# Performance work log

Measured on AMD Instinct MI355X. Metric: run time of the kernel, lower is better.

Reference implementation:

```python
import jax, jax.numpy as jnp
import numpy as np

B, TZ, TU = 32, 16, 128
E, H, V = 512, 1024, 32000
FREQ_THRES = 4   # cfg.freq_thres: zero out copy prob for most-frequent tokens
LN_EPS = 1e-3


def setup_inputs() -> dict:
    key = jax.random.key(0)
    ks = jax.random.split(key, 16)
    s = lambda k, shape, sc=0.02: jax.random.normal(k, shape, jnp.float32) * sc
    return dict(
        z_enc_out=jax.random.normal(ks[0], (TZ, B, H), jnp.float32),
        pz_proba=jax.nn.softmax(jax.random.normal(ks[1], (TZ, B, V), jnp.float32), axis=-1),
        u_enc_out=jax.random.normal(ks[2], (TU, B, H), jnp.float32),
        m_t_input=jax.random.randint(ks[3], (1, B), 0, V),
        last_hidden=jax.random.normal(ks[4], (1, B, H), jnp.float32),
        emb=s(ks[5], (V, E), 1.0 / np.sqrt(E)),
        Wa_z=s(ks[6], (2 * H, H)), ba_z=jnp.zeros((H,), jnp.float32), v_z=s(ks[7], (H,), 1.0 / np.sqrt(H)),
        Wa_u=s(ks[8], (2 * H, H)), ba_u=jnp.zeros((H,), jnp.float32), v_u=s(ks[9], (H,), 1.0 / np.sqrt(H)),
        W_ih=s(ks[10], (3 * H, E + 2 * H)), W_hh=s(ks[11], (3 * H, H)),
        b_ih=jnp.zeros((3 * H,), jnp.float32), b_hh=jnp.zeros((3 * H,), jnp.float32),
        ln_a=jnp.ones((H,), jnp.float32), ln_b=jnp.zeros((H,), jnp.float32),
        W_proj=s(ks[12], (H, V)), b_proj=jnp.zeros((V,), jnp.float32),
        W_c=s(ks[13], (2 * H, H)), b_c=jnp.zeros((H,), jnp.float32),
        W_v1=s(ks[14], (H, 1)), b_v1=jnp.zeros((1,), jnp.float32),
    )


def _attn(hidden, enc, Wa, ba, v):
    # hidden [1,B,H], enc [T,B,H] -> context [1,B,H]
    hh = jnp.broadcast_to(hidden, enc.shape)                       # [T,B,H]
    energy = jnp.tanh(jnp.concatenate([hh, enc], -1) @ Wa + ba)    # [T,B,H]
    scores = jnp.einsum('tbh,h->bt', energy, v)                    # [B,T]
    w = jax.nn.softmax(scores, axis=1)
    return jnp.einsum('bt,tbh->bh', w, enc)[None]                  # [1,B,H]


def _layernorm(x, a, b):
    mu = jnp.mean(x, axis=-1, keepdims=True)
    sigma = jnp.std(x, axis=-1, keepdims=True, ddof=1)  # torch.std is unbiased
    return (x - mu) / (sigma + LN_EPS) * a + b


def reference(z_enc_out, pz_proba, u_enc_out, m_t_input, last_hidden,
              emb, Wa_z, ba_z, v_z, Wa_u, ba_u, v_u,
              W_ih, W_hh, b_ih, b_hh, ln_a, ln_b,
              W_proj, b_proj, W_c, b_c, W_v1, b_v1):
    m_embed = emb[m_t_input]                                       # [1,B,E]
    z_ctx = _attn(last_hidden, z_enc_out, Wa_z, ba_z, v_z)         # [1,B,H]
    u_ctx = _attn(last_hidden, u_enc_out, Wa_u, ba_u, v_u)         # [1,B,H]
    x = jnp.concatenate([z_ctx, u_ctx, m_embed], -1)[0]            # [B,2H+E]
    h = last_hidden[0]                                             # [B,H]
    # single-step GRU (torch gate order: r, z, n)
    gi = x @ W_ih.T + b_ih
    gh = h @ W_hh.T + b_hh
    ir, iz, inn = jnp.split(gi, 3, axis=-1)
    hr, hz, hn = jnp.split(gh, 3, axis=-1)
    r = jax.nn.sigmoid(ir + hr)
    zg = jax.nn.sigmoid(iz + hz)
    n = jnp.tanh(inn + r * hn)
    h_new = (1.0 - zg) * n + zg * h                                # [B,H]
    gru_out = _layernorm(h_new, ln_a, ln_b)                        # [B,H]
    gen_score = gru_out @ W_proj + b_proj                          # [B,V]
    # tanh-linear copy score over z positions
    g_rep = jnp.broadcast_to(gru_out[None], z_enc_out.shape)       # [Tz,B,H]
    zc = jnp.tanh(jnp.concatenate([z_enc_out, g_rep], -1) @ W_c + b_c)  # [Tz,B,H]
    zc = (zc @ W_v1 + b_v1)[..., 0].T                              # [B,Tz]
    # joint softmax over [gen | copy]
    scores = jax.nn.softmax(jnp.concatenate([gen_score, zc], axis=1), axis=1)
    gen_p, copy_p = scores[:, :V], scores[:, V:]
    copy_v = jnp.einsum('bt,tbv->bv', copy_p, pz_proba)            # mask_prob bmm
    freq_mask = (jnp.arange(V) >= FREQ_THRES).astype(gen_p.dtype)
    proba = gen_p + copy_v * freq_mask
    return proba, h_new[None]
```

## Files before the change

kernel.cpp:

```cpp
#include <hip/hip_runtime.h>
#include <stdint.h>

#define B_ 32
#define TZ_ 16
#define TU_ 128
#define E_ 512
#define H_ 1024
#define V_ 32000
#define X_ 2560
#define H3_ 3072
#define LN_EPS_ 0.001f

#define NP_IH 20
#define NP_HH 16

typedef unsigned short ushort_t;
typedef ushort_t us4 __attribute__((ext_vector_type(4)));
typedef ushort_t us8 __attribute__((ext_vector_type(8)));
typedef short bf16x8 __attribute__((ext_vector_type(8)));
typedef float f32x4 __attribute__((ext_vector_type(4)));

__device__ __forceinline__ float bf2f(ushort_t u){
  union { unsigned int i; float f; } x; x.i = ((unsigned int)u) << 16; return x.f;
}
__device__ __forceinline__ ushort_t f2b(float f){
  union { float f; unsigned int i; } u; u.f = f;
  unsigned int x = u.i;
  return (ushort_t)((x + 0x7fffu + ((x >> 16) & 1u)) >> 16);
}
__device__ __forceinline__ bool is_bf(const void* lnA){
  return *(const unsigned int*)lnA == 0x3F803F80u;
}
__device__ __forceinline__ float ldg_(const void* p, size_t i, bool isb){
  return isb ? bf2f(((const ushort_t*)p)[i]) : ((const float*)p)[i];
}
__device__ __forceinline__ float sigm(float x){ return 1.0f/(1.0f + __expf(-x)); }
__device__ __forceinline__ float tanh_f(float x){
  float cx = fminf(fmaxf(x, -9.0f), 9.0f);
  float t = __expf(2.0f*cx);
  return (t - 1.0f)/(t + 1.0f);
}

__global__ void k0_init(const void* lh, const void* emb, const int* mt,
                        const void* ba_z, const void* ba_u, const void* b_c, const void* bpj,
                        const void* lnA,
                        float* h_f32, ushort_t* hb, float* x, float* hWaZ, float* hWaU,
                        float* sz, float* su, float* gruWc, float* genscore){
  bool isb = is_bf(lnA);
  int i = blockIdx.x*256 + threadIdx.x;
  if (i < 32768){ float v = ldg_(lh, i, isb); h_f32[i] = v; hb[i] = f2b(v); return; }
  i -= 32768;
  if (i < 16384){ int b = i >> 9, e = i & 511;
    x[b*X_ + 2048 + e] = ldg_(emb, (size_t)(unsigned)mt[b]*E_ + e, isb); return; }
  i -= 16384;
  if (i < 32768){ hWaZ[i] = ldg_(ba_z, i & 1023, isb); return; }
  i -= 32768;
  if (i < 32768){ hWaU[i] = ldg_(ba_u, i & 1023, isb); return; }
  i -= 32768;
  if (i < 4608){ if (i < 512) sz[i] = 0.f; else su[i-512] = 0.f; return; }
  i -= 4608;
  if (i < 32768){ gruWc[i] = ldg_(b_c, i & 1023, isb); return; }
  i -= 32768;
  if (i < 1024000){
    int b = i / V_;
    int v = i - b*V_;
    genscore[(size_t)b*V_ + v] = ldg_(bpj, v, isb);
    return;
  }
}

__global__ void kC_cvt(const void* uenc, const void* zenc, const void* Wih, const void* Whh,
                       const void* lnA,
                       ushort_t* uB, ushort_t* zB, ushort_t* WihB, ushort_t* WhhB){
  bool isb = is_bf(lnA);
  long long i = (long long)(blockIdx.x*256 + threadIdx.x) * 8;
  const long long NU = (long long)TU_*B_*H_;
  const long long NZ = (long long)TZ_*B_*H_;
  const long long NI = (long long)H3_*X_;
  const long long NH = (long long)H3_*H_;
  const void* src; ushort_t* dst;
  if (i < NU){ src = uenc; dst = uB; }
  else if ((i -= NU) < NZ){ src = zenc; dst = zB; }
  else if ((i -= NZ) < NI){ src = Wih; dst = WihB; }
  else if ((i -= NI) < NH){ src = Whh; dst = WhhB; }
  else return;
  if (isb){
    *(us8*)&dst[i] = *(const us8*)((const ushort_t*)src + i);
  } else {
    const float* s = (const float*)src + i;
    float4 a0 = *(const float4*)s, a1 = *(const float4*)(s + 4);
    us8 o;
    o[0]=f2b(a0.x); o[1]=f2b(a0.y); o[2]=f2b(a0.z); o[3]=f2b(a0.w);
    o[4]=f2b(a1.x); o[5]=f2b(a1.y); o[6]=f2b(a1.z); o[7]=f2b(a1.w);
    *(us8*)&dst[i] = o;
  }
}

__global__ void kX_cvt(const float* x, ushort_t* xb){
  int i = (blockIdx.x*256 + threadIdx.x) * 8;
  const float* s = x + i;
  float4 a0 = *(const float4*)s, a1 = *(const float4*)(s + 4);
  us8 o;
  o[0]=f2b(a0.x); o[1]=f2b(a0.y); o[2]=f2b(a0.z); o[3]=f2b(a0.w);
  o[4]=f2b(a1.x); o[5]=f2b(a1.y); o[6]=f2b(a1.z); o[7]=f2b(a1.w);
  *(us8*)&xb[i] = o;
}

__global__ void kT_transpose(const void* Wz, const void* Wu, const void* Wc, const void* lnA,
                             ushort_t* tZ, ushort_t* tU, ushort_t* tC){
  bool isb = is_bf(lnA);
  int w = blockIdx.z;
  const void* src = (w==0)? Wz : (w==1)? Wu : Wc;
  size_t base = (w==2) ? 0 : (size_t)H_*H_;
  ushort_t* dst = (w==0)? tZ : (w==1)? tU : tC;
  __shared__ ushort_t T[64][68];
  int k0 = blockIdx.x*64, j0 = blockIdx.y*64;
  int tx = threadIdx.x & 15, ty = threadIdx.x >> 4;
  if (isb){
    const ushort_t* s = (const ushort_t*)src + base;
    #pragma unroll
    for (int rr=0; rr<4; ++rr){
      int row = ty + rr*16;
      *(us4*)&T[row][tx*4] = *(const us4*)&s[(size_t)(k0+row)*H_ + j0 + tx*4];
    }
  } else {
    const float* s = (const float*)src + base;
    #pragma unroll
    for (int rr=0; rr<4; ++rr){
      int row = ty + rr*16;
      #pragma unroll
      for (int c=0;c<4;c++)
        T[row][tx*4+c] = f2b(s[(size_t)(k0+row)*H_ + j0 + tx*4 + c]);
    }
  }
  __syncthreads();
  #pragma unroll
  for (int rr=0; rr<4; ++rr){
    int row = ty + rr*16;
    us4 o;
    o[0]=T[tx*4+0][row]; o[1]=T[tx*4+1][row]; o[2]=T[tx*4+2][row]; o[3]=T[tx*4+3][row];
    *(us4*)&dst[(size_t)(j0+row)*H_ + k0 + tx*4] = o;
  }
}

__global__ void k1_kj(const float* xf, const void* W0, const void* W1, int eloff, const void* lnA,
                      float* out0, float* out1){
  bool isb = is_bf(lnA);
  const void* W = blockIdx.z ? W1 : W0;
  float* out = blockIdx.z ? out1 : out0;
  int j = blockIdx.x*256 + threadIdx.x;
  int k0v = blockIdx.y*64;
  float acc[32];
  #pragma unroll
  for (int b=0;b<32;b++) acc[b]=0.f;
  if (isb){
    const ushort_t* Wp = (const ushort_t*)W + eloff;
    #pragma unroll 4
    for (int k=k0v; k<k0v+64; ++k){
      float w = bf2f(Wp[(size_t)k*H_ + j]);
      #pragma unroll
      for (int b=0;b<32;b++) acc[b] = fmaf(xf[b*H_ + k], w, acc[b]);
    }
  } else {
    const float* Wp = (const float*)W + eloff;
    #pragma unroll 4
    for (int k=k0v; k<k0v+64; ++k){
      float w = Wp[(size_t)k*H_ + j];
      #pragma unroll
      for (int b=0;b<32;b++) acc[b] = fmaf(xf[b*H_ + k], w, acc[b]);
    }
  }
  #pragma unroll
  for (int b=0;b<32;b++) unsafeAtomicAdd(&out[b*H_ + j], acc[b]);
}

__global__ __launch_bounds__(256) void k2_mfma(const ushort_t* Ab, const ushort_t* WB,
                                               float* part, int K, int kchunk){
  int j0 = blockIdx.x*128;
  int kb = blockIdx.y*kchunk;
  __shared__ ushort_t Bs[128*32];
  int tid = threadIdx.x, wid = tid >> 6, lane = tid & 63;
  int q = lane >> 4, n = lane & 15;
  int rrow = tid >> 2, t4 = tid & 3;
  f32x4 acc[2][2];
  #pragma unroll
  for (int r=0;r<2;r++)
    #pragma unroll
    for (int c=0;c<2;c++)
      #pragma unroll
      for (int e=0;e<4;e++) acc[r][c][e] = 0.f;

  for (int kt = 0; kt < kchunk; kt += 32){
    int k = kb + kt;
    __syncthreads();
    #pragma unroll
    for (int p=0;p<2;p++){
      const ushort_t* srcB = WB + (size_t)(j0 + p*64 + rrow)*K + k + t4*8;
      __builtin_amdgcn_global_load_lds(srcB, &Bs[(p*64 + wid*16)*32], 16, 0, 0);
    }
    __syncthreads();
    bf16x8 af[2], bfr[2];
    #pragma unroll
    for (int r=0;r<2;r++) af[r] = *(const bf16x8*)&Ab[(size_t)(r*16 + n)*K + k + q*8];
    #pragma unroll
    for (int c=0;c<2;c++) bfr[c] = *(const bf16x8*)&Bs[(wid*32 + c*16 + n)*32 + q*8];
    #pragma unroll
    for (int r=0;r<2;r++)
      #pragma unroll
      for (int c=0;c<2;c++)
        acc[r][c] = __builtin_amdgcn_mfma_f32_16x16x32_bf16(af[r], bfr[c], acc[r][c], 0, 0, 0);
  }
  int p = blockIdx.y;
  #pragma unroll
  for (int r=0;r<2;r++)
    #pragma unroll
    for (int c=0;c<2;c++)
      #pragma unroll
      for (int i=0;i<4;i++){
        int b = r*16 + q*4 + i;
        int j = j0 + wid*32 + c*16 + n;
        part[(size_t)(p*32 + b)*H3_ + j] = acc[r][c][i];
      }
}

__global__ __launch_bounds__(256) void k3_mfma(
    const ushort_t* uB, const ushort_t* zB,
    const ushort_t* tU, const ushort_t* tZ, const ushort_t* tC,
    const float* hWaU, const float* hWaZ,
    const void* v_u, const void* v_z, const void* lnA,
    float* su, float* sz, float* zcpre)
{
  bool isb = is_bf(lnA);
  int which = blockIdx.z;
  int bx = blockIdx.x, nt = blockIdx.y;
  int mt;
  const ushort_t* A; const ushort_t* BT;
  if (which == 0){ A = uB; BT = tU; mt = bx; }
  else {
    int lo = (which==1) ? 8 : 12;
    if (bx < lo || bx >= lo+4) return;
    mt = bx - lo;
    A = zB; BT = (which==1) ? tZ : tC;
  }
  __shared__ ushort_t As[128*32];
  __shared__ ushort_t Bs[64*32];
  int tid = threadIdx.x;
  int wid = tid >> 6, lane = tid & 63;
  int q = lane >> 4, n = lane & 15;
  int wm = wid & 1, wn = wid >> 1;
  int r0 = mt*128, j0 = nt*64;
  f32x4 acc[4][2];
  #pragma unroll
  for (int a=0;a<4;a++)
    #pragma unroll
    for (int c=0;c<2;c++)
      #pragma unroll
      for (int e=0;e<4;e++) acc[a][c][e] = 0.f;

  int rrow = tid >> 2, t4 = tid & 3;

  for (int kt = 0; kt < 32; ++kt){
    __syncthreads();
    #pragma unroll
    for (int p=0;p<2;p++){
      const ushort_t* srcA = A + (size_t)(r0 + p*64 + rrow)*H_ + kt*32 + t4*8;
      __builtin_amdgcn_global_load_lds(srcA, &As[(p*64 + wid*16)*32], 16, 0, 0);
    }
    {
      const ushort_t* srcB = BT + (size_t)(j0 + rrow)*H_ + kt*32 + t4*8;
      __builtin_amdgcn_global_load_lds(srcB, &Bs[(wid*16)*32], 16, 0, 0);
    }
    __syncthreads();
    bf16x8 af[4], bfr[2];
    #pragma unroll
    for (int f=0;f<4;f++) af[f] = *(const bf16x8*)&As[(wm*64 + f*16 + n)*32 + q*8];
    #pragma unroll
    for (int f=0;f<2;f++) bfr[f] = *(const bf16x8*)&Bs[(wn*32 + f*16 + n)*32 + q*8];
    #pragma unroll
    for (int fr=0;fr<4;fr++)
      #pragma unroll
      for (int fn=0;fn<2;fn++)
        acc[fr][fn] = __builtin_amdgcn_mfma_f32_16x16x32_bf16(af[fr], bfr[fn], acc[fr][fn], 0, 0, 0);
  }

  if (which < 2){
    const float* pre = (which==0) ? hWaU : hWaZ;
    const void* vv = (which==0) ? v_u : v_z;
    float* score = (which==0) ? su : sz;
    float s[4][4];
    #pragma unroll
    for (int fr=0;fr<4;fr++)
      #pragma unroll
      for (int i=0;i<4;i++) s[fr][i]=0.f;
    #pragma unroll
    for (int fr=0;fr<4;fr++){
      #pragma unroll
      for (int fn=0;fn<2;fn++){
        int j  = j0 + wn*32 + fn*16 + n;
        float vj = ldg_(vv, j, isb);
        #pragma unroll
        for (int i=0;i<4;i++){
          int rl = wm*64 + fr*16 + q*4 + i;
          int b  = rl & 31;
          s[fr][i] += tanh_f(acc[fr][fn][i] + pre[b*H_ + j]) * vj;
        }
      }
    }
    #pragma unroll
    for (int fr=0;fr<4;fr++)
      #pragma unroll
      for (int i=0;i<4;i++){
        float t = s[fr][i];
        t += __shfl_xor(t, 1);
        t += __shfl_xor(t, 2);
        t += __shfl_xor(t, 4);
        t += __shfl_xor(t, 8);
        if (n == 0){
          int rl = wm*64 + fr*16 + q*4 + i;
          unsafeAtomicAdd(&score[r0 + rl], t);
        }
      }
  } else {
    #pragma unroll
    for (int fr=0;fr<4;fr++)
      #pragma unroll
      for (int fn=0;fn<2;fn++)
        #pragma unroll
        for (int i=0;i<4;i++){
          int rl = wm*64 + fr*16 + q*4 + i;
          int jl = wn*32 + fn*16 + n;
          zcpre[(size_t)(r0 + rl)*H_ + j0 + jl] = acc[fr][fn][i];
        }
  }
}

__global__ void k4_ctx(const float* sz, const float* su,
                       const void* zenc, const void* uenc, const void* lnA, float* x){
  bool isb = is_bf(lnA);
  int jc = blockIdx.x, b = blockIdx.y, which = blockIdx.z;
  int T = which ? TU_ : TZ_;
  const float* sc = which ? su : sz;
  const void* enc = which ? uenc : zenc;
  __shared__ float red[256];
  __shared__ float w[TU_];
  int tid = threadIdx.x;
  float v = (tid < T) ? sc[tid*B_ + b] : -1e30f;
  red[tid] = v; __syncthreads();
  for (int s=128; s>0; s>>=1){ if (tid < s) red[tid] = fmaxf(red[tid], red[tid+s]); __syncthreads(); }
  float m = red[0]; __syncthreads();
  float e = (tid < T) ? __expf(v - m) : 0.f;
  red[tid] = e; __syncthreads();
  for (int s=128; s>0; s>>=1){ if (tid < s) red[tid] += red[tid+s]; __syncthreads(); }
  float S = red[0]; __syncthreads();
  if (tid < T) w[tid] = e / S;
  __syncthreads();
  int j = jc*256 + tid;
  float acc = 0.f;
  #pragma unroll 4
  for (int t=0; t<T; ++t) acc = fmaf(w[t], ldg_(enc, (size_t)(t*B_ + b)*H_ + j, isb), acc);
  x[b*X_ + which*H_ + j] = acc;
}

__global__ __launch_bounds__(1024) void k5_gru(const float* gip, const float* ghp,
                       const void* b_ih, const void* b_hh,
                       const void* lh, const void* ln_a, const void* ln_b,
                       float* gru, float* hout){
  bool isb = is_bf(ln_a);
  int b = blockIdx.x, tid = threadIdx.x;
  __shared__ float red[1024];
  int j = tid;
  float ir = ldg_(b_ih, j, isb), iz = ldg_(b_ih, 1024+j, isb), inn = ldg_(b_ih, 2048+j, isb);
  float hr = ldg_(b_hh, j, isb), hz = ldg_(b_hh, 1024+j, isb), hn = ldg_(b_hh, 2048+j, isb);
  #pragma unroll 4
  for (int p=0;p<NP_IH;p++){
    const float* gp = &gip[(size_t)(p*32 + b)*H3_];
    ir += gp[j]; iz += gp[1024+j]; inn += gp[2048+j];
  }
  #pragma unroll 4
  for (int p=0;p<NP_HH;p++){
    const float* gp = &ghp[(size_t)(p*32 + b)*H3_];
    hr += gp[j]; hz += gp[1024+j]; hn += gp[2048+j];
  }
  float hv = ldg_(lh, b*H_ + j, isb);
  float r  = sigm(ir + hr);
  float zg = sigm(iz + hz);
  float nn = tanh_f(inn + r*hn);
  float h2 = (1.f - zg)*nn + zg*hv;
  hout[b*H_ + j] = h2;
  red[tid] = h2; __syncthreads();
  for (int s=512;s>0;s>>=1){ if(tid<s) red[tid]+=red[tid+s]; __syncthreads(); }
  float mu = red[0] / 1024.f; __syncthreads();
  red[tid] = h2*h2; __syncthreads();
  for (int s=512;s>0;s>>=1){ if(tid<s) red[tid]+=red[tid+s]; __syncthreads(); }
  float var = (red[0] - 1024.f*mu*mu) / 1023.f;
  float sg = sqrtf(fmaxf(var, 0.f));
  float inv = 1.f/(sg + LN_EPS_);
  gru[b*H_ + j] = (h2 - mu)*inv*ldg_(ln_a, j, isb) + ldg_(ln_b, j, isb);
}

__global__ void k7_zc(const float* zcpre, const float* gruWc, const void* Wv1,
                      const void* b_v1, const void* lnA, float* zc){
  bool isb = is_bf(lnA);
  int r = blockIdx.x, b = r & 31, tid = threadIdx.x;
  __shared__ float red[256];
  float s = 0.f;
  #pragma unroll
  for (int jj=0;jj<4;jj++){
    int j = tid + jj*256;
    float e = tanh_f(zcpre[(size_t)r*H_ + j] + gruWc[b*H_ + j]);
    s = fmaf(e, ldg_(Wv1, j, isb), s);
  }
  red[tid] = s; __syncthreads();
  for (int st=128;st>0;st>>=1){ if(tid<st) red[tid]+=red[tid+st]; __syncthreads(); }
  if (tid==0) zc[r] = red[0] + ldg_(b_v1, 0, isb);
}

__global__ __launch_bounds__(256) void k6_proj(const float* gru, const void* Wp,
                                               const void* lnA, float* genscore){
  bool isb = is_bf(lnA);
  int v = blockIdx.x*256 + threadIdx.x;
  int h0 = blockIdx.y*128;
  float acc[32];
  #pragma unroll
  for (int b=0;b<32;b++) acc[b]=0.f;
  if (isb){
    const ushort_t* W = (const ushort_t*)Wp;
    #pragma unroll 4
    for (int h=h0; h<h0+128; ++h){
      float w = bf2f(W[(size_t)h*V_ + v]);
      #pragma unroll
      for (int b=0;b<32;b++) acc[b] = fmaf(gru[b*H_ + h], w, acc[b]);
    }
  } else {
    const float* W = (const float*)Wp;
    #pragma unroll 4
    for (int h=h0; h<h0+128; ++h){
      float w = W[(size_t)h*V_ + v];
      #pragma unroll
      for (int b=0;b<32;b++) acc[b] = fmaf(gru[b*H_ + h], w, acc[b]);
    }
  }
  #pragma unroll
  for (int b=0;b<32;b++) unsafeAtomicAdd(&genscore[(size_t)b*V_ + v], acc[b]);
}

__global__ void k8a(const float* genscore, float* statpart){
  int v = blockIdx.x*256 + threadIdx.x;
  int b = blockIdx.y, tid = threadIdx.x;
  __shared__ float red[256];
  float g = genscore[(size_t)b*V_ + v];
  red[tid] = g; __syncthreads();
  for (int s=128;s>0;s>>=1){ if(tid<s) red[tid]=fmaxf(red[tid],red[tid+s]); __syncthreads(); }
  float m = red[0]; __syncthreads();
  float e = __expf(g - m);
  red[tid] = e; __syncthreads();
  for (int s=128;s>0;s>>=1){ if(tid<s) red[tid]+=red[tid+s]; __syncthreads(); }
  if (tid==0){ statpart[(b*125 + blockIdx.x)*2] = m; statpart[(b*125 + blockIdx.x)*2+1] = red[0]; }
}

__global__ void k8b(const float* statpart, const float* zc, float* stats, float* copyp){
  int b = blockIdx.x, tid = threadIdx.x;
  __shared__ float red[128];
  float m = -1e30f, s = 0.f;
  if (tid < 125){ m = statpart[(b*125 + tid)*2]; s = statpart[(b*125 + tid)*2 + 1]; }
  float zv = (tid < 16) ? zc[tid*B_ + b] : -1e30f;
  red[tid] = fmaxf(m, zv); __syncthreads();
  for (int st=64;st>0;st>>=1){ if(tid<st) red[tid]=fmaxf(red[tid],red[tid+st]); __syncthreads(); }
  float M = red[0]; __syncthreads();
  float zp = (tid < 125) ? s*__expf(m - M) : 0.f;
  if (tid < 16) zp += __expf(zv - M);
  red[tid] = zp; __syncthreads();
  for (int st=64;st>0;st>>=1){ if(tid<st) red[tid]+=red[tid+st]; __syncthreads(); }
  float invZ = 1.f/red[0];
  if (tid < 16) copyp[b*16 + tid] = __expf(zv - M)*invZ;
  if (tid == 0){ stats[b*2] = M; stats[b*2+1] = invZ; }
}

__global__ void k8c(const float* genscore, const float* stats, const float* copyp,
                    const void* pz, const void* lnA, float* out){
  bool isb = is_bf(lnA);
  int v = blockIdx.x*256 + threadIdx.x;
  int b = blockIdx.y;
  float M = stats[b*2], invZ = stats[b*2+1];
  float p = __expf(genscore[(size_t)b*V_ + v] - M)*invZ;
  if (v >= 4){
    float cv = 0.f;
    if (isb){
      const ushort_t* pzp = (const ushort_t*)pz;
      #pragma unroll
      for (int t=0;t<16;t++)
        cv = fmaf(copyp[b*16 + t], bf2f(pzp[(size_t)(t*B_ + b)*V_ + v]), cv);
    } else {
      const float* pzp = (const float*)pz;
      #pragma unroll
      for (int t=0;t<16;t++)
        cv = fmaf(copyp[b*16 + t], pzp[(size_t)(t*B_ + b)*V_ + v], cv);
    }
    p += cv;
  }
  out[(size_t)b*V_ + v] = p;
}

extern "C" void kernel_launch(void* const* d_in, const int* in_sizes, int n_in,
                              void* d_out, int out_size, void* d_ws, size_t ws_size,
                              hipStream_t stream){
  const void* z_enc = d_in[0];
  const void* pz    = d_in[1];
  const void* u_enc = d_in[2];
  const int*  m_t   = (const int*)d_in[3];
  const void* lh    = d_in[4];
  const void* emb   = d_in[5];
  const void* Wa_z  = d_in[6];
  const void* ba_z  = d_in[7];
  const void* v_z   = d_in[8];
  const void* Wa_u  = d_in[9];
  const void* ba_u  = d_in[10];
  const void* v_u   = d_in[11];
  const void* W_ih  = d_in[12];
  const void* W_hh  = d_in[13];
  const void* b_ih  = d_in[14];
  const void* b_hh  = d_in[15];
  const void* ln_a  = d_in[16];
  const void* ln_b  = d_in[17];
  const void* W_proj= d_in[18];
  const void* b_proj= d_in[19];
  const void* W_c   = d_in[20];
  const void* b_c   = d_in[21];
  const void* W_v1  = d_in[22];
  const void* b_v1  = d_in[23];

  float* wsf = (float*)d_ws;
  size_t o = 0;
  auto alloc = [&](size_t n){ float* p = wsf + o; o += n; return p; };
  float* h_f32 = alloc(B_*H_);
  float* x     = alloc(B_*X_);
  float* hWaZ  = alloc(B_*H_);
  float* hWaU  = alloc(B_*H_);
  float* sz    = alloc(TZ_*B_);
  float* su    = alloc(TU_*B_);
  float* gru   = alloc(B_*H_);
  float* gruWc = alloc(B_*H_);
  float* zcpre = alloc((size_t)TZ_*B_*H_);
  float* zcv   = alloc(TZ_*B_);
  float* ghp   = alloc((size_t)NP_HH*B_*H3_);
  float* gip   = alloc((size_t)NP_IH*B_*H3_);
  float* genscore = alloc((size_t)B_*V_);
  float* statpart = alloc(B_*125*2);
  float* stats = alloc(B_*2);
  float* copyp = alloc(B_*TZ_);
  o = (o + 7) & ~(size_t)7;
  ushort_t* wT = (ushort_t*)(wsf + o);
  ushort_t* tZ = wT;
  ushort_t* tU = wT + (size_t)H_*H_;
  ushort_t* tC = wT + (size_t)2*H_*H_;
  o += (size_t)3*H_*H_/2;
  ushort_t* uB = (ushort_t*)(wsf + o);
  o += (size_t)TU_*B_*H_/2;
  ushort_t* zB = (ushort_t*)(wsf + o);
  o += (size_t)TZ_*B_*H_/2;
  ushort_t* WihB = (ushort_t*)(wsf + o);
  o += (size_t)H3_*X_/2;
  ushort_t* WhhB = (ushort_t*)(wsf + o);
  o += (size_t)H3_*H_/2;
  ushort_t* xb = (ushort_t*)(wsf + o);
  o += (size_t)B_*X_/2;
  ushort_t* hb = (ushort_t*)(wsf + o);
  o += (size_t)B_*H_/2;
  float* outp = (float*)d_out;
  float* hout = outp + (size_t)B_*V_;

  k0_init<<<4594, 256, 0, stream>>>(lh, emb, m_t, ba_z, ba_u, b_c, b_proj, ln_a,
                                    h_f32, hb, x, hWaZ, hWaU, sz, su, gruWc, genscore);
  kC_cvt<<<7680, 256, 0, stream>>>(u_enc, z_enc, W_ih, W_hh, ln_a, uB, zB, WihB, WhhB);
  kT_transpose<<<dim3(16,16,3), 256, 0, stream>>>(Wa_z, Wa_u, W_c, ln_a, tZ, tU, tC);
  k1_kj<<<dim3(4,16,2), 256, 0, stream>>>(h_f32, Wa_z, Wa_u, 0, ln_a, hWaZ, hWaU);
  k2_mfma<<<dim3(24,NP_HH), 256, 0, stream>>>(hb, WhhB, ghp, H_, 64);
  k3_mfma<<<dim3(32,16,3), 256, 0, stream>>>(uB, zB, tU, tZ, tC, hWaU, hWaZ, v_u, v_z, ln_a, su, sz, zcpre);
  k4_ctx<<<dim3(4,32,2), 256, 0, stream>>>(sz, su, z_enc, u_enc, ln_a, x);
  kX_cvt<<<40, 256, 0, stream>>>(x, xb);
  k2_mfma<<<dim3(24,NP_IH), 256, 0, stream>>>(xb, WihB, gip, X_, 128);
  k5_gru<<<32, 1024, 0, stream>>>(gip, ghp, b_ih, b_hh, lh, ln_a, ln_b, gru, hout);
  k1_kj<<<dim3(4,16,1), 256, 0, stream>>>(gru, W_c, W_c, H_*H_, ln_a, gruWc, gruWc);
  k7_zc<<<512, 256, 0, stream>>>(zcpre, gruWc, W_v1, b_v1, ln_a, zcv);
  k6_proj<<<dim3(125,8), 256, 0, stream>>>(gru, W_proj, ln_a, genscore);
  k8a<<<dim3(125,32), 256, 0, stream>>>(genscore, statpart);
  k8b<<<32, 128, 0, stream>>>(statpart, zcv, stats, copyp);
  k8c<<<dim3(125,32), 256, 0, stream>>>(genscore, stats, copyp, pz, ln_a, outp);
}
```

Baseline: 523.1 us.

## Replace scalar vocab projection with bf16 MFMA kernel over pre-transposed W_proj

Adds a kernel that transposes and converts W_proj into a bf16 [V,H] buffer each call, has the GRU kernel also emit a bf16 copy of the layernormed output, and replaces the scalar FMA projection kernel with an MFMA 16x16x32 bf16 kernel that atomically accumulates K-split partials into genscore. The goal is to move the largest GEMM onto matrix cores and off scalar FP32 FMAs. It adds a full extra read and write pass over the 32000x1024 weight every call and lowers the activations to bf16 precision.

```diff
diff --git a/kernel.cpp b/kernel.cpp
--- a/kernel.cpp
+++ b/kernel.cpp
@@ -143,6 +143,38 @@
   }
 }
 
+__global__ void kP_t(const void* Wp, const void* lnA, ushort_t* WpT){
+  bool isb = is_bf(lnA);
+  __shared__ ushort_t T[64][68];
+  int h0 = blockIdx.x*64, v0 = blockIdx.y*64;
+  int tx = threadIdx.x & 15, ty = threadIdx.x >> 4;
+  if (isb){
+    const ushort_t* s = (const ushort_t*)Wp;
+    #pragma unroll
+    for (int rr=0; rr<4; ++rr){
+      int row = ty + rr*16;
+      *(us4*)&T[row][tx*4] = *(const us4*)&s[(size_t)(h0+row)*V_ + v0 + tx*4];
+    }
+  } else {
+    const float* s = (const float*)Wp;
+    #pragma unroll
+    for (int rr=0; rr<4; ++rr){
+      int row = ty + rr*16;
+      #pragma unroll
+      for (int c=0;c<4;c++)
+        T[row][tx*4+c] = f2b(s[(size_t)(h0+row)*V_ + v0 + tx*4 + c]);
+    }
+  }
+  __syncthreads();
+  #pragma unroll
+  for (int rr=0; rr<4; ++rr){
+    int row = ty + rr*16;
+    us4 o;
+    o[0]=T[tx*4+0][row]; o[1]=T[tx*4+1][row]; o[2]=T[tx*4+2][row]; o[3]=T[tx*4+3][row];
+    *(us4*)&WpT[(size_t)(v0+row)*H_ + h0 + tx*4] = o;
+  }
+}
+
 __global__ void k1_kj(const float* xf, const void* W0, const void* W1, int eloff, const void* lnA,
                       float* out0, float* out1){
   bool isb = is_bf(lnA);
@@ -220,6 +252,54 @@
         int b = r*16 + q*4 + i;
         int j = j0 + wid*32 + c*16 + n;
         part[(size_t)(p*32 + b)*H3_ + j] = acc[r][c][i];
+      }
+}
+
+__global__ __launch_bounds__(256) void k6_mfma(const ushort_t* grub, const ushort_t* WpT,
+                                               float* genscore){
+  int j0 = blockIdx.x*128;
+  int kb = blockIdx.y*256;
+  __shared__ ushort_t Bs[128*32];
+  int tid = threadIdx.x, wid = tid >> 6, lane = tid & 63;
+  int q = lane >> 4, n = lane & 15;
+  int rrow = tid >> 2, t4 = tid & 3;
+  f32x4 acc[2][2];
+  #pragma unroll
+  for (int r=0;r<2;r++)
+    #pragma unroll
+    for (int c=0;c<2;c++)
+      #pragma unroll
+      for (int e=0;e<4;e++) acc[r][c][e] = 0.f;
+
+  for (int kt = 0; kt < 256; kt += 32){
+    int k = kb + kt;
+    __syncthreads();
+    #pragma unroll
+    for (int p=0;p<2;p++){
+      const ushort_t* srcB = WpT + (size_t)(j0 + p*64 + rrow)*H_ + k + t4*8;
+      __builtin_amdgcn_global_load_lds(srcB, &Bs[(p*64 + wid*16)*32], 16, 0, 0);
+    }
+    __syncthreads();
+    bf16x8 af[2], bfr[2];
+    #pragma unroll
+    for (int r=0;r<2;r++) af[r] = *(const bf16x8*)&grub[(size_t)(r*16 + n)*H_ + k + q*8];
+    #pragma unroll
+    for (int c=0;c<2;c++) bfr[c] = *(const bf16x8*)&Bs[(wid*32 + c*16 + n)*32 + q*8];
+    #pragma unroll
+    for (int r=0;r<2;r++)
+      #pragma unroll
+      for (int c=0;c<2;c++)
+        acc[r][c] = __builtin_amdgcn_mfma_f32_16x16x32_bf16(af[r], bfr[c], acc[r][c], 0, 0, 0);
+  }
+  #pragma unroll
+  for (int r=0;r<2;r++)
+    #pragma unroll
+    for (int c=0;c<2;c++)
+      #pragma unroll
+      for (int i=0;i<4;i++){
+        int b = r*16 + q*4 + i;
+        int v = j0 + wid*32 + c*16 + n;
+        unsafeAtomicAdd(&genscore[(size_t)b*V_ + v], acc[r][c][i]);
       }
 }
 
@@ -364,7 +444,7 @@
 __global__ __launch_bounds__(1024) void k5_gru(const float* gip, const float* ghp,
                        const void* b_ih, const void* b_hh,
                        const void* lh, const void* ln_a, const void* ln_b,
-                       float* gru, float* hout){
+                       float* gru, ushort_t* grub, float* hout){
   bool isb = is_bf(ln_a);
   int b = blockIdx.x, tid = threadIdx.x;
   __shared__ float red[1024];
@@ -395,7 +475,9 @@
   float var = (red[0] - 1024.f*mu*mu) / 1023.f;
   float sg = sqrtf(fmaxf(var, 0.f));
   float inv = 1.f/(sg + LN_EPS_);
-  gru[b*H_ + j] = (h2 - mu)*inv*ldg_(ln_a, j, isb) + ldg_(ln_b, j, isb);
+  float g = (h2 - mu)*inv*ldg_(ln_a, j, isb) + ldg_(ln_b, j, isb);
+  gru[b*H_ + j] = g;
+  grub[b*H_ + j] = f2b(g);
 }
 
 __global__ void k7_zc(const float* zcpre, const float* gruWc, const void* Wv1,
@@ -413,35 +495,6 @@
   red[tid] = s; __syncthreads();
   for (int st=128;st>0;st>>=1){ if(tid<st) red[tid]+=red[tid+st]; __syncthreads(); }
   if (tid==0) zc[r] = red[0] + ldg_(b_v1, 0, isb);
-}
-
-__global__ __launch_bounds__(256) void k6_proj(const float* gru, const void* Wp,
-                                               const void* lnA, float* genscore){
-  bool isb = is_bf(lnA);
-  int v = blockIdx.x*256 + threadIdx.x;
-  int h0 = blockIdx.y*128;
-  float acc[32];
-  #pragma unroll
-  for (int b=0;b<32;b++) acc[b]=0.f;
-  if (isb){
-    const ushort_t* W = (const ushort_t*)Wp;
-    #pragma unroll 4
-    for (int h=h0; h<h0+128; ++h){
-      float w = bf2f(W[(size_t)h*V_ + v]);
-      #pragma unroll
-      for (int b=0;b<32;b++) acc[b] = fmaf(gru[b*H_ + h], w, acc[b]);
-    }
-  } else {
-    const float* W = (const float*)Wp;
-    #pragma unroll 4
-    for (int h=h0; h<h0+128; ++h){
-      float w = W[(size_t)h*V_ + v];
-      #pragma unroll
-      for (int b=0;b<32;b++) acc[b] = fmaf(gru[b*H_ + h], w, acc[b]);
-    }
-  }
-  #pragma unroll
-  for (int b=0;b<32;b++) unsafeAtomicAdd(&genscore[(size_t)b*V_ + v], acc[b]);
 }
 
 __global__ void k8a(const float* genscore, float* statpart){
@@ -566,12 +619,17 @@
   o += (size_t)B_*X_/2;
   ushort_t* hb = (ushort_t*)(wsf + o);
   o += (size_t)B_*H_/2;
+  ushort_t* grub = (ushort_t*)(wsf + o);
+  o += (size_t)B_*H_/2;
+  ushort_t* WpT = (ushort_t*)(wsf + o);
+  o += (size_t)V_*H_/2;
   float* outp = (float*)d_out;
   float* hout = outp + (size_t)B_*V_;
 
   k0_init<<<4594, 256, 0, stream>>>(lh, emb, m_t, ba_z, ba_u, b_c, b_proj, ln_a,
                                     h_f32, hb, x, hWaZ, hWaU, sz, su, gruWc, genscore);
   kC_cvt<<<7680, 256, 0, stream>>>(u_enc, z_enc, W_ih, W_hh, ln_a, uB, zB, WihB, WhhB);
+  kP_t<<<dim3(16,500), 256, 0, stream>>>(W_proj, ln_a, WpT);
   kT_transpose<<<dim3(16,16,3), 256, 0, stream>>>(Wa_z, Wa_u, W_c, ln_a, tZ, tU, tC);
   k1_kj<<<dim3(4,16,2), 256, 0, stream>>>(h_f32, Wa_z, Wa_u, 0, ln_a, hWaZ, hWaU);
   k2_mfma<<<dim3(24,NP_HH), 256, 0, stream>>>(hb, WhhB, ghp, H_, 64);
@@ -579,10 +637,10 @@
   k4_ctx<<<dim3(4,32,2), 256, 0, stream>>>(sz, su, z_enc, u_enc, ln_a, x);
   kX_cvt<<<40, 256, 0, stream>>>(x, xb);
   k2_mfma<<<dim3(24,NP_IH), 256, 0, stream>>>(xb, WihB, gip, X_, 128);
-  k5_gru<<<32, 1024, 0, stream>>>(gip, ghp, b_ih, b_hh, lh, ln_a, ln_b, gru, hout);
+  k5_gru<<<32, 1024, 0, stream>>>(gip, ghp, b_ih, b_hh, lh, ln_a, ln_b, gru, grub, hout);
   k1_kj<<<dim3(4,16,1), 256, 0, stream>>>(gru, W_c, W_c, H_*H_, ln_a, gruWc, gruWc);
   k7_zc<<<512, 256, 0, stream>>>(zcpre, gruWc, W_v1, b_v1, ln_a, zcv);
-  k6_proj<<<dim3(125,8), 256, 0, stream>>>(gru, W_proj, ln_a, genscore);
+  k6_mfma<<<dim3(250,4), 256, 0, stream>>>(grub, WpT, genscore);
   k8a<<<dim3(125,32), 256, 0, stream>>>(genscore, statpart);
   k8b<<<32, 128, 0, stream>>>(statpart, zcv, stats, copyp);
   k8c<<<dim3(125,32), 256, 0, stream>>>(genscore, stats, copyp, pz, ln_a, outp);
```

Measured after the change: 550.1 us. 1.05x slower.
